# Kernel tuning notes

Measured on AMD Instinct MI355X. Metric: run time of the kernel, lower is better.

The kernel has to match this reference:

```python
import jax, jax.numpy as jnp
import numpy as np

B, N, D = 2, 8192, 64          # batch, points, feature dim (dim_in == dim_out)
FILTER_SIZE = 11               # k nearest neighbors in feature space
N_ITER = 5                     # mean-field iterations


def setup_inputs() -> dict:
    key = jax.random.key(0)
    k0, k1, k2, k3 = jax.random.split(key, 4)
    return {
        "logits": jax.random.normal(k0, (B, N), jnp.float32),
        "p": jax.random.normal(k1, (B, D, N), jnp.float32),
        "W1": jax.random.normal(k2, (D, D), jnp.float32) / np.float32(np.sqrt(D)),
        "b1": jnp.zeros((D,), jnp.float32),
        "W2": jax.random.normal(k3, (D, D), jnp.float32) / np.float32(np.sqrt(D)),
        "b2": jnp.zeros((D,), jnp.float32),
    }


def reference(logits, p, W1, b1, W2, b2):
    # crf_encoder: two stacked Linear layers applied to p.permute(0,2,1) -> [B,N,D]
    f = jnp.einsum('bdn,de->bne', p, W1) + b1
    f = jnp.einsum('bne,ef->bnf', f, W2) + b2  # [B,N,D] feature embedding

    # pairwise squared distances in feature space: [B,N,N]
    sq = jnp.sum(f * f, axis=-1)
    d2 = sq[:, :, None] + sq[:, None, :] - 2.0 * jnp.einsum('bnd,bmd->bnm', f, f)

    # filter_size nearest neighbors (includes self) with Gaussian weights exp(-d2)
    neg_d2, idx = jax.lax.top_k(-d2, FILTER_SIZE)   # [B,N,K]
    w = jnp.exp(neg_d2)                             # [B,N,K]

    gather = jax.vmap(lambda qb, ib: qb[ib])        # per-batch gather: [N],[N,K]->[N,K]

    # mean-field iterations (binary CRF: sigmoid marginals, unary = logits)
    u = logits
    for _ in range(N_ITER):
        q = jax.nn.sigmoid(u)                       # current marginals [B,N]
        msg = jnp.sum(w * gather(q, idx), axis=-1)  # filtered message   [B,N]
        u = logits - msg                            # compatibility transform + unary

    return jax.nn.sigmoid(u)  # return_log_proba=False -> probabilities, [B,N]
```

## Files before the change

### kernel.cpp

```cpp
#include <hip/hip_runtime.h>

#define NPTS 8192
#define NTOT 16384
#define KNB 11
#define CAP 16
#define MARG 9.0f

typedef __attribute__((ext_vector_type(8))) short short8;
typedef __attribute__((ext_vector_type(4))) float f32x4;

__device__ __forceinline__ unsigned short f2bf(float x) {
  union { float f; unsigned u; } v; v.f = x;
  unsigned r = v.u + 0x7FFFu + ((v.u >> 16) & 1u);
  return (unsigned short)(r >> 16);
}

__device__ __forceinline__ float sigm(float x) { return 1.f / (1.f + expf(-x)); }

__global__ __launch_bounds__(512) void k1_encode(
    const float* __restrict__ p,
    const float* __restrict__ W1, const float* __restrict__ b1,
    const float* __restrict__ W2, const float* __restrict__ b2,
    float* __restrict__ f32f,
    unsigned short* __restrict__ fpre,
    float* __restrict__ sq,
    float* __restrict__ sq32,
    unsigned* __restrict__ cnt) {
  __shared__ float sW1[64 * 65];
  __shared__ float sW2[64 * 64];
  __shared__ float sW12[64 * 64];
  __shared__ float sb[64];
  __shared__ float sPart[8][64];
  int t = threadIdx.x;
  int gid = blockIdx.x * 512 + t;
  if (gid < NTOT) cnt[gid] = 0u;

  for (int i = t; i < 4096; i += 512) {
    sW1[(i >> 6) * 65 + (i & 63)] = W1[i];
    sW2[i] = W2[i];
  }
  __syncthreads();

  {
    int d = t >> 3, e0c = (t & 7) * 8;
    float a8[8];
#pragma unroll
    for (int j = 0; j < 8; ++j) a8[j] = 0.f;
    for (int k = 0; k < 64; ++k) {
      float a = sW1[d * 65 + k];
#pragma unroll
      for (int j = 0; j < 8; ++j)
        a8[j] = fmaf(a, sW2[k * 64 + e0c + j], a8[j]);
    }
#pragma unroll
    for (int j = 0; j < 8; ++j) sW12[d * 64 + e0c + j] = a8[j];
  }
  if (t < 64) {
    float sbv = b2[t];
    for (int k = 0; k < 64; ++k) sbv = fmaf(b1[k], sW2[k * 64 + t], sbv);
    sb[t] = sbv;
  }
  __syncthreads();

  int lane = t & 63;
  int w = __builtin_amdgcn_readfirstlane(t >> 6);
  int e0 = w * 8;
  int base = blockIdx.x * 64;
  int b = base >> 13, n0 = base & (NPTS - 1);
  const float* pb = p + (size_t)b * 64 * NPTS + n0 + lane;

  float f[8];
#pragma unroll
  for (int j = 0; j < 8; ++j) f[j] = sb[e0 + j];
#pragma unroll 8
  for (int d = 0; d < 64; ++d) {
    float pd = pb[(size_t)d * NPTS];
#pragma unroll
    for (int j = 0; j < 8; ++j)
      f[j] = fmaf(pd, sW12[d * 64 + e0 + j], f[j]);
  }
  float s = 0.f;
#pragma unroll
  for (int j = 0; j < 8; ++j) s = fmaf(f[j], f[j], s);
  sPart[w][lane] = s;
  __syncthreads();
  if (w == 0) {
    float s32 = (sPart[0][lane] + sPart[1][lane]) + (sPart[2][lane] + sPart[3][lane]);
    float s64 = s32 + ((sPart[4][lane] + sPart[5][lane]) + (sPart[6][lane] + sPart[7][lane]));
    sq32[base + lane] = s32;
    sq[base + lane] = s64;
  }
  f32x4* o4 = (f32x4*)(f32f + (size_t)(base + lane) * 64 + e0);
  { f32x4 v0; v0[0]=f[0]; v0[1]=f[1]; v0[2]=f[2]; v0[3]=f[3]; o4[0]=v0;
    f32x4 v1; v1[0]=f[4]; v1[1]=f[5]; v1[2]=f[6]; v1[3]=f[7]; o4[1]=v1; }
  if (w < 4) {
    unsigned* ob = (unsigned*)(fpre + (size_t)(base + lane) * 32 + e0);
#pragma unroll
    for (int jj = 0; jj < 4; ++jj) {
      unsigned lo = f2bf(f[2 * jj]);
      unsigned hi = f2bf(f[2 * jj + 1]);
      ob[jj] = lo | (hi << 16);
    }
  }
}

__global__ __launch_bounds__(256) void k2_gram_select(
    const unsigned short* __restrict__ fpre,
    const float* __restrict__ sq32,
    unsigned* __restrict__ cnt,
    unsigned* __restrict__ cand) {
  __shared__ uint4 sB[1024];
  int bid = blockIdx.x;
  int b = (bid >= 528) ? 1 : 0;
  int rem = bid - b * 528;
  int band = (int)((sqrtf(8.f * (float)rem + 1.f) - 1.f) * 0.5f);
  if (((band + 1) * (band + 2)) / 2 <= rem) band++;
  else if ((band * (band + 1)) / 2 > rem) band--;
  int seg = rem - (band * (band + 1)) / 2;

  int t = threadIdx.x;
  int lane = t & 63, wave = t >> 6;
  int arow = lane & 15;
  int q = lane >> 4;
  int rowbase = band * 256 + wave * 64;
  int cbase = seg * 256;
  const unsigned short* fb = fpre + (size_t)b * NPTS * 32;
  const float* s32b = sq32 + b * NPTS;

  const uint4* gsrc = (const uint4*)fb + (size_t)seg * 1024;
  uint4 v[4];
#pragma unroll
  for (int k = 0; k < 4; ++k) v[k] = gsrc[t + k * 256];

  short8 afrag[4];
#pragma unroll
  for (int tr = 0; tr < 4; ++tr)
    afrag[tr] = *(const short8*)(fb + (size_t)(rowbase + tr * 16 + arow) * 32 + q * 8);

  f32x4 srq[4];
  float hs0, hs1, hs2, hs3;
#pragma unroll
  for (int tr = 0; tr < 4; ++tr)
    srq[tr] = *(const f32x4*)(s32b + rowbase + tr * 16 + (q << 2));
  hs0 = 0.5f * fminf(fminf(srq[0][0], srq[0][1]), fminf(srq[0][2], srq[0][3]));
  hs1 = 0.5f * fminf(fminf(srq[1][0], srq[1][1]), fminf(srq[1][2], srq[1][3]));
  hs2 = 0.5f * fminf(fminf(srq[2][0], srq[2][1]), fminf(srq[2][2], srq[2][3]));
  hs3 = 0.5f * fminf(fminf(srq[3][0], srq[3][1]), fminf(srq[3][2], srq[3][3]));

  float scq[16];
#pragma unroll
  for (int cc = 0; cc < 4; ++cc)
#pragma unroll
    for (int tc = 0; tc < 4; ++tc)
      scq[cc * 4 + tc] = s32b[cbase + cc * 64 + tc * 16 + arow];

#pragma unroll
  for (int k = 0; k < 4; ++k) {
    int c = t + k * 256;
    int r = c >> 2, qq = c & 3;
    sB[r * 4 + (qq ^ (r & 3))] = v[k];
  }
  __syncthreads();

  f32x4 z4 = {0.f, 0.f, 0.f, 0.f};
  float cm = -1e30f;
#pragma unroll
  for (int cc = 0; cc < 4; ++cc)
#pragma unroll
    for (int tc = 0; tc < 4; ++tc) {
      int rl = cc * 64 + tc * 16 + arow;
      short8 bf = *(const short8*)&sB[rl * 4 + (q ^ (rl & 3))];
      f32x4 a0 = __builtin_amdgcn_mfma_f32_16x16x32_bf16(afrag[0], bf, z4, 0, 0, 0);
      f32x4 a1 = __builtin_amdgcn_mfma_f32_16x16x32_bf16(afrag[1], bf, z4, 0, 0, 0);
      f32x4 a2 = __builtin_amdgcn_mfma_f32_16x16x32_bf16(afrag[2], bf, z4, 0, 0, 0);
      f32x4 a3 = __builtin_amdgcn_mfma_f32_16x16x32_bf16(afrag[3], bf, z4, 0, 0, 0);
      float t0 = fmaxf(fmaxf(a0[0], a0[1]), fmaxf(a0[2], a0[3])) - hs0;
      float t1 = fmaxf(fmaxf(a1[0], a1[1]), fmaxf(a1[2], a1[3])) - hs1;
      float t2 = fmaxf(fmaxf(a2[0], a2[1]), fmaxf(a2[2], a2[3])) - hs2;
      float t3 = fmaxf(fmaxf(a3[0], a3[1]), fmaxf(a3[2], a3[3])) - hs3;
      float m = fmaxf(fmaxf(t0, t1), fmaxf(t2, t3));
      cm = fmaxf(cm, m - 0.5f * scq[cc * 4 + tc]);
    }

  if (__ballot(cm > -0.5f * MARG)) {
#pragma unroll 1
    for (int cc = 0; cc < 4; ++cc)
#pragma unroll 1
      for (int tc = 0; tc < 4; ++tc) {
        int rl = cc * 64 + tc * 16 + arow;
        short8 bf = *(const short8*)&sB[rl * 4 + (q ^ (rl & 3))];
        int colpt = cbase + cc * 64 + tc * 16 + arow;
        float scv = s32b[colpt];
#pragma unroll
        for (int tr = 0; tr < 4; ++tr) {
          f32x4 a = __builtin_amdgcn_mfma_f32_16x16x32_bf16(afrag[tr], bf, z4, 0, 0, 0);
#pragma unroll
          for (int rg = 0; rg < 4; ++rg) {
            float d2 = srq[tr][rg] + scv - 2.f * a[rg];
            if (d2 < MARG) {
              int rowpt = rowbase + tr * 16 + (q << 2) + rg;
              int gr = b * NPTS + rowpt;
              union { float f; unsigned u; } cv; cv.f = d2 + 16.f;
              unsigned kb = cv.u & 0xFFFFE000u;
              unsigned slot = atomicAdd(&cnt[gr], 1u);
              if (slot < CAP) cand[gr * CAP + slot] = kb | (unsigned)colpt;
              if (band != seg) {
                int gc = b * NPTS + colpt;
                unsigned slot2 = atomicAdd(&cnt[gc], 1u);
                if (slot2 < CAP) cand[gc * CAP + slot2] = kb | (unsigned)rowpt;
              }
            }
          }
        }
      }
  }
}

__global__ __launch_bounds__(256) void k3_refine(
    const float* __restrict__ f32f, const float* __restrict__ sq,
    const unsigned* __restrict__ cnt, const unsigned* __restrict__ cand,
    float* __restrict__ W, int* __restrict__ IDX) {
  int r = blockIdx.x * 256 + threadIdx.x;
  int b = r >> 13;
  unsigned count = cnt[r];
  if (count > CAP) count = CAP;
  if (count <= 1) return;

  unsigned k[CAP];
#pragma unroll
  for (int j = 0; j < CAP; ++j)
    k[j] = (j < (int)count) ? cand[r * CAP + j] : 0xFFFFFFFFu;
#pragma unroll
  for (int a = 0; a < CAP - 1; ++a)
#pragma unroll
    for (int c = 0; c < CAP - 1; ++c) {
      unsigned lo = min(k[c], k[c + 1]);
      unsigned hi = max(k[c], k[c + 1]);
      k[c] = lo; k[c + 1] = hi;
    }

  float fr[64];
  const f32x4* fr4 = (const f32x4*)(f32f + (size_t)r * 64);
#pragma unroll
  for (int j = 0; j < 16; ++j) {
    f32x4 v = fr4[j];
    fr[4 * j] = v[0]; fr[4 * j + 1] = v[1]; fr[4 * j + 2] = v[2]; fr[4 * j + 3] = v[3];
  }
  float sqr = sq[r];
  int nsel = (int)count < KNB ? (int)count : KNB;
#pragma unroll
  for (int kk = 0; kk < KNB; ++kk) {
    float w = 0.f;
    int gi = r;
    if (kk < nsel) {
      int col = (int)(k[kk] & 8191u);
      gi = b * NPTS + col;
      const float* fm = f32f + (size_t)gi * 64;
      float dot = 0.f;
#pragma unroll
      for (int d = 0; d < 64; ++d) dot = fmaf(fr[d], fm[d], dot);
      float d2 = sqr + sq[gi] - 2.f * dot;
      w = expf(-d2);
    }
    W[r * KNB + kk] = w;
    IDX[r * KNB + kk] = gi;
  }
}

__global__ __launch_bounds__(1024) void k4_fused(
    const float* __restrict__ logits, const unsigned* __restrict__ cnt,
    const float* __restrict__ W, const int* __restrict__ IDX,
    float* __restrict__ out) {
  __shared__ float qs[NPTS];
  int t = threadIdx.x;
  int rb = blockIdx.x * NPTS;
  float lg[8], u[8];
  unsigned c[8];
#pragma unroll
  for (int j = 0; j < 8; ++j) {
    int il = j * 1024 + t;
    lg[j] = logits[rb + il];
    c[j] = cnt[rb + il];
    u[j] = lg[j];
    qs[il] = sigm(u[j]);
  }
  __syncthreads();
  for (int it = 0; it < 5; ++it) {
#pragma unroll
    for (int j = 0; j < 8; ++j) {
      int il = j * 1024 + t;
      float msg;
      if (c[j] <= 1u) {
        msg = qs[il];
      } else {
        msg = 0.f;
        const float* wp = W + (size_t)(rb + il) * KNB;
        const int* ip = IDX + (size_t)(rb + il) * KNB;
#pragma unroll
        for (int kk = 0; kk < KNB; ++kk) msg = fmaf(wp[kk], qs[ip[kk] - rb], msg);
      }
      u[j] = lg[j] - msg;
    }
    __syncthreads();
#pragma unroll
    for (int j = 0; j < 8; ++j) qs[j * 1024 + t] = sigm(u[j]);
    __syncthreads();
  }
#pragma unroll
  for (int j = 0; j < 8; ++j) out[rb + j * 1024 + t] = sigm(u[j]);
}

extern "C" void kernel_launch(void* const* d_in, const int* in_sizes, int n_in,
                              void* d_out, int out_size, void* d_ws, size_t ws_size,
                              hipStream_t stream) {
  const float* logits = (const float*)d_in[0];
  const float* p      = (const float*)d_in[1];
  const float* W1     = (const float*)d_in[2];
  const float* b1     = (const float*)d_in[3];
  const float* W2     = (const float*)d_in[4];
  const float* b2     = (const float*)d_in[5];
  float* out = (float*)d_out;

  char* ws = (char*)d_ws;
  float* f32f = (float*)ws;
  unsigned short* fpre = (unsigned short*)(f32f + (size_t)NTOT * 64);
  float* sq = (float*)(fpre + (size_t)NTOT * 32);
  float* sq32 = sq + NTOT;
  unsigned* cnt = (unsigned*)(sq32 + NTOT);
  unsigned* cand = cnt + NTOT;
  float* Wbuf = (float*)(cand + (size_t)NTOT * CAP);
  int* IDX = (int*)(Wbuf + (size_t)NTOT * KNB);

  k1_encode<<<256, 512, 0, stream>>>(p, W1, b1, W2, b2, f32f, fpre, sq, sq32, cnt);
  k2_gram_select<<<1056, 256, 0, stream>>>(fpre, sq32, cnt, cand);
  k3_refine<<<64, 256, 0, stream>>>(f32f, sq, cnt, cand, Wbuf, IDX);
  k4_fused<<<2, 1024, 0, stream>>>(logits, cnt, Wbuf, IDX, out);
}
```

Before: 133.4 us.

## Precompute fused W1·W2 once in a separate kernel instead of per block

Moves the W1·W2 product and combined bias computation out of the encode kernel into a small dedicated kernel, so each of the 256 encode blocks no longer redundantly loads both weight matrices and recomputes the 64x64 product in shared memory. The encode kernel now uses 256 threads, each producing 16 output features, and reads the fused weights from global memory (wave-uniform, cache resident). This adds an extra kernel launch and global reads of W12 in the inner loop in exchange for removing per-block redundant setup work and shared memory usage.

```diff
diff --git a/kernel.cpp b/kernel.cpp
--- a/kernel.cpp
+++ b/kernel.cpp
@@ -17,86 +17,75 @@
 
 __device__ __forceinline__ float sigm(float x) { return 1.f / (1.f + expf(-x)); }
 
-__global__ __launch_bounds__(512) void k1_encode(
-    const float* __restrict__ p,
+__global__ __launch_bounds__(256) void k0_w12(
     const float* __restrict__ W1, const float* __restrict__ b1,
     const float* __restrict__ W2, const float* __restrict__ b2,
+    float* __restrict__ W12, float* __restrict__ b12,
+    unsigned* __restrict__ cnt) {
+  int t = blockIdx.x * 256 + threadIdx.x;
+  cnt[t] = 0u;
+  if (t >= 4096) return;
+  int d = t >> 6, e = t & 63;
+  float s = 0.f;
+  for (int kk = 0; kk < 64; ++kk) s = fmaf(W1[d * 64 + kk], W2[kk * 64 + e], s);
+  W12[t] = s;
+  if (d == 0) {
+    float sb = b2[e];
+    for (int kk = 0; kk < 64; ++kk) sb = fmaf(b1[kk], W2[kk * 64 + e], sb);
+    b12[e] = sb;
+  }
+}
+
+__global__ __launch_bounds__(256) void k1_encode(
+    const float* __restrict__ p,
+    const float* __restrict__ W12,
+    const float* __restrict__ b12,
     float* __restrict__ f32f,
     unsigned short* __restrict__ fpre,
     float* __restrict__ sq,
-    float* __restrict__ sq32,
-    unsigned* __restrict__ cnt) {
-  __shared__ float sW1[64 * 65];
-  __shared__ float sW2[64 * 64];
-  __shared__ float sW12[64 * 64];
-  __shared__ float sb[64];
-  __shared__ float sPart[8][64];
-  int t = threadIdx.x;
-  int gid = blockIdx.x * 512 + t;
-  if (gid < NTOT) cnt[gid] = 0u;
-
-  for (int i = t; i < 4096; i += 512) {
-    sW1[(i >> 6) * 65 + (i & 63)] = W1[i];
-    sW2[i] = W2[i];
-  }
-  __syncthreads();
-
-  {
-    int d = t >> 3, e0c = (t & 7) * 8;
-    float a8[8];
-#pragma unroll
-    for (int j = 0; j < 8; ++j) a8[j] = 0.f;
-    for (int k = 0; k < 64; ++k) {
-      float a = sW1[d * 65 + k];
-#pragma unroll
-      for (int j = 0; j < 8; ++j)
-        a8[j] = fmaf(a, sW2[k * 64 + e0c + j], a8[j]);
-    }
-#pragma unroll
-    for (int j = 0; j < 8; ++j) sW12[d * 64 + e0c + j] = a8[j];
-  }
-  if (t < 64) {
-    float sbv = b2[t];
-    for (int k = 0; k < 64; ++k) sbv = fmaf(b1[k], sW2[k * 64 + t], sbv);
-    sb[t] = sbv;
-  }
-  __syncthreads();
-
-  int lane = t & 63;
+    float* __restrict__ sq32) {
+  __shared__ float sPart[4][64];
+  int t = threadIdx.x, lane = t & 63;
   int w = __builtin_amdgcn_readfirstlane(t >> 6);
-  int e0 = w * 8;
+  int e0 = w * 16;
   int base = blockIdx.x * 64;
   int b = base >> 13, n0 = base & (NPTS - 1);
   const float* pb = p + (size_t)b * 64 * NPTS + n0 + lane;
 
-  float f[8];
-#pragma unroll
-  for (int j = 0; j < 8; ++j) f[j] = sb[e0 + j];
+  float f[16];
+#pragma unroll
+  for (int j = 0; j < 16; ++j) f[j] = b12[e0 + j];
+
 #pragma unroll 8
   for (int d = 0; d < 64; ++d) {
     float pd = pb[(size_t)d * NPTS];
 #pragma unroll
-    for (int j = 0; j < 8; ++j)
-      f[j] = fmaf(pd, sW12[d * 64 + e0 + j], f[j]);
-  }
+    for (int j = 0; j < 16; ++j)
+      f[j] = fmaf(pd, W12[d * 64 + e0 + j], f[j]);
+  }
+
   float s = 0.f;
 #pragma unroll
-  for (int j = 0; j < 8; ++j) s = fmaf(f[j], f[j], s);
+  for (int j = 0; j < 16; ++j) s = fmaf(f[j], f[j], s);
   sPart[w][lane] = s;
   __syncthreads();
   if (w == 0) {
-    float s32 = (sPart[0][lane] + sPart[1][lane]) + (sPart[2][lane] + sPart[3][lane]);
-    float s64 = s32 + ((sPart[4][lane] + sPart[5][lane]) + (sPart[6][lane] + sPart[7][lane]));
+    float s32 = sPart[0][lane] + sPart[1][lane];
+    float s64 = s32 + (sPart[2][lane] + sPart[3][lane]);
     sq32[base + lane] = s32;
     sq[base + lane] = s64;
   }
+
   f32x4* o4 = (f32x4*)(f32f + (size_t)(base + lane) * 64 + e0);
-  { f32x4 v0; v0[0]=f[0]; v0[1]=f[1]; v0[2]=f[2]; v0[3]=f[3]; o4[0]=v0;
-    f32x4 v1; v1[0]=f[4]; v1[1]=f[5]; v1[2]=f[6]; v1[3]=f[7]; o4[1]=v1; }
-  if (w < 4) {
+#pragma unroll
+  for (int jj = 0; jj < 4; ++jj) {
+    f32x4 v; v[0] = f[4 * jj]; v[1] = f[4 * jj + 1]; v[2] = f[4 * jj + 2]; v[3] = f[4 * jj + 3];
+    o4[jj] = v;
+  }
+  if (w < 2) {
     unsigned* ob = (unsigned*)(fpre + (size_t)(base + lane) * 32 + e0);
 #pragma unroll
-    for (int jj = 0; jj < 4; ++jj) {
+    for (int jj = 0; jj < 8; ++jj) {
       unsigned lo = f2bf(f[2 * jj]);
       unsigned hi = f2bf(f[2 * jj + 1]);
       ob[jj] = lo | (hi << 16);
@@ -322,7 +311,9 @@
   float* out = (float*)d_out;
 
   char* ws = (char*)d_ws;
-  float* f32f = (float*)ws;
+  float* W12 = (float*)ws;
+  float* b12 = W12 + 4096;
+  float* f32f = b12 + 64;
   unsigned short* fpre = (unsigned short*)(f32f + (size_t)NTOT * 64);
   float* sq = (float*)(fpre + (size_t)NTOT * 32);
   float* sq32 = sq + NTOT;
@@ -331,7 +322,8 @@
   float* Wbuf = (float*)(cand + (size_t)NTOT * CAP);
   int* IDX = (int*)(Wbuf + (size_t)NTOT * KNB);
 
-  k1_encode<<<256, 512, 0, stream>>>(p, W1, b1, W2, b2, f32f, fpre, sq, sq32, cnt);
+  k0_w12<<<64, 256, 0, stream>>>(W1, b1, W2, b2, W12, b12, cnt);
+  k1_encode<<<256, 256, 0, stream>>>(p, W12, b12, f32f, fpre, sq, sq32);
   k2_gram_select<<<1056, 256, 0, stream>>>(fpre, sq32, cnt, cand);
   k3_refine<<<64, 256, 0, stream>>>(f32f, sq, cnt, cand, Wbuf, IDX);
   k4_fused<<<2, 1024, 0, stream>>>(logits, cnt, Wbuf, IDX, out);
```

After: 140.9 us. 1.06x slower.
